# Performance work log

Hardware: AMD Instinct MI355X
Metric: run time of the kernel (lower is better)

The kernel has to match this reference:

```python
import jax, jax.numpy as jnp
import numpy as np

NUM_USERS = 60000
NUM_ITEMS = 40000
NUM_NODES = NUM_USERS + NUM_ITEMS
EMB = 64
HID = 32
N_EDGES = 1600000
BATCH = 16384


def setup_inputs() -> dict:
    key = jax.random.key(0)
    ks = jax.random.split(key, 16)
    def xavier(k, shape):
        fan_in, fan_out = shape[1], shape[0]
        lim = float(np.sqrt(6.0 / (fan_in + fan_out)))
        return jax.random.uniform(k, shape, jnp.float32, -lim, lim)
    return {
        "user_ids": jax.random.randint(ks[0], (BATCH,), 0, NUM_USERS),
        "item_ids": jax.random.randint(ks[1], (BATCH,), 0, NUM_ITEMS),
        "adj_rows": jax.random.randint(ks[2], (N_EDGES,), 0, NUM_NODES),
        "adj_cols": jax.random.randint(ks[3], (N_EDGES,), 0, NUM_NODES),
        "adj_vals": jax.random.uniform(ks[4], (N_EDGES,), jnp.float32),
        # embeddings (xavier_uniform, matching init_weights)
        "user_emb_w": xavier(ks[5], (NUM_USERS, EMB)),
        "item_emb_w": xavier(ks[6], (NUM_ITEMS, EMB)),
        # GC layer 1: 64 -> 32 ; GC layer 2: 32 -> 64
        "gc1_w": xavier(ks[7], (HID, EMB)),
        "gc1_b": jnp.zeros((HID,), jnp.float32),
        "gc2_w": xavier(ks[8], (EMB, HID)),
        "gc2_b": jnp.zeros((EMB,), jnp.float32),
        # predictor: Linear(2*EMB -> HID), ReLU, Linear(HID -> 1), Sigmoid
        "p1_w": xavier(ks[9], (HID, 2 * EMB)),
        "p1_b": jnp.zeros((HID,), jnp.float32),
        "p2_w": xavier(ks[10], (1, HID)),
        "p2_b": jnp.zeros((1,), jnp.float32),
    }


def _gc_layer(x, rows, cols, vals, w, b):
    # dense linear then spmm: out[i] = sum_e vals[e] * h[cols[e]] grouped by rows[e]
    h = x @ w.T + b                                # [N, out_dim]
    msg = vals[:, None] * h[cols]                  # [E, out_dim] gather (memory-bound)
    agg = jax.ops.segment_sum(msg, rows, num_segments=NUM_NODES)
    return jax.nn.relu(agg)                        # dropout in eval mode = identity


def reference(user_ids, item_ids, adj_rows, adj_cols, adj_vals,
              user_emb_w, item_emb_w, gc1_w, gc1_b, gc2_w, gc2_b,
              p1_w, p1_b, p2_w, p2_b):
    node_feat = jnp.concatenate([user_emb_w, item_emb_w], axis=0)  # [N, EMB]
    h = _gc_layer(node_feat, adj_rows, adj_cols, adj_vals, gc1_w, gc1_b)
    h = _gc_layer(h, adj_rows, adj_cols, adj_vals, gc2_w, gc2_b)
    final_user_emb = h[:NUM_USERS]
    final_item_emb = h[NUM_USERS:]
    bu = final_user_emb[user_ids]                  # [B, EMB]
    bi = final_item_emb[item_ids]                  # [B, EMB]
    z = jnp.concatenate([bu, bi], axis=1)          # [B, 2*EMB]
    z = jax.nn.relu(z @ p1_w.T + p1_b)             # [B, HID]
    scores = jax.nn.sigmoid(z @ p2_w.T + p2_b).squeeze(-1)  # [B]
    return (scores, final_user_emb, final_item_emb)
```

## Files before the change

### kernel.cpp

```cpp
#include <hip/hip_runtime.h>
#include <hip/hip_bf16.h>

#define NUM_USERS 60000
#define NUM_ITEMS 40000
#define NUM_NODES 100000
#define EMB 64
#define HID 32
#define N_EDGES 1600000
#define BATCH 16384

#define TILE 128
#define NBUCK 782
#define CAPB 3072
#define BLOCK_E 4096
#define NBLK_A 391
#define EPT 8
#define EPT_B (CAPB / 256)

#define WS_CUR    0
#define WS_BEND   800
#define WS_ROFF   1600
#define WS_BINNED 101952
#define WS_H1     4906560
#define WS_G      8106560
#define WS_SUMV   11306560

__global__ __launch_bounds__(1024) void k_initcur(unsigned* __restrict__ cur)
{
    int t = threadIdx.x;
    if (t < NBUCK) cur[t] = (unsigned)t * CAPB;
}

__global__ __launch_bounds__(512) void k_partA(
    const int* __restrict__ rows, const int* __restrict__ cols,
    const float* __restrict__ vals,
    unsigned* __restrict__ cursor, uint2* __restrict__ binned)
{
    __shared__ unsigned cnt[NBUCK];
    __shared__ unsigned offs[NBUCK];
    __shared__ unsigned gbase[NBUCK];
    __shared__ unsigned scanbuf[1024];
    __shared__ uint2    staged[BLOCK_E];
    __shared__ unsigned dstarr[BLOCK_E];

    int t = threadIdx.x;
    for (int i = t; i < NBUCK; i += 512) cnt[i] = 0u;
    __syncthreads();

    unsigned eb = blockIdx.x * BLOCK_E;
    unsigned bb[EPT], rk[EPT];
    uint2    pr[EPT];
    #pragma unroll
    for (int i = 0; i < EPT; i++) {
        unsigned e = eb + (unsigned)(i * 512 + t);
        if (e < N_EDGES) {
            unsigned r = (unsigned)rows[e];
            bb[i] = r >> 7;
            pr[i] = make_uint2(((r & 127u) << 17) | (unsigned)cols[e],
                               __float_as_uint(vals[e]));
            rk[i] = atomicAdd(&cnt[bb[i]], 1u);
        } else {
            bb[i] = 0xFFFFFFFFu;
        }
    }
    __syncthreads();

    unsigned c0 = (t < NBUCK) ? cnt[t] : 0u;
    unsigned c1 = (t + 512 < NBUCK) ? cnt[t + 512] : 0u;
    scanbuf[t] = c0; scanbuf[t + 512] = c1;
    __syncthreads();
    #pragma unroll
    for (int ofs = 1; ofs < 1024; ofs <<= 1) {
        unsigned a0 = (t >= ofs) ? scanbuf[t - ofs] : 0u;
        unsigned a1 = (t + 512 >= ofs) ? scanbuf[t + 512 - ofs] : 0u;
        __syncthreads();
        scanbuf[t] += a0; scanbuf[t + 512] += a1;
        __syncthreads();
    }
    if (t < NBUCK) offs[t] = scanbuf[t] - c0;
    if (t + 512 < NBUCK) offs[t + 512] = scanbuf[t + 512] - c1;
    __syncthreads();

    for (int b = t; b < NBUCK; b += 512) {
        unsigned c = cnt[b];
        gbase[b] = c ? atomicAdd(&cursor[b], c) : 0u;
    }
    __syncthreads();

    #pragma unroll
    for (int i = 0; i < EPT; i++) {
        if (bb[i] != 0xFFFFFFFFu) {
            unsigned s = offs[bb[i]] + rk[i];
            staged[s] = pr[i];
            dstarr[s] = gbase[bb[i]] + rk[i];
        }
    }
    __syncthreads();

    unsigned total = (eb + BLOCK_E <= N_EDGES) ? (unsigned)BLOCK_E
                                               : (N_EDGES - eb);
    for (unsigned s = t; s < total; s += 512)
        binned[dstarr[s]] = staged[s];
}

__global__ __launch_bounds__(256) void k_partB(
    const unsigned* __restrict__ cursor,
    uint2* __restrict__ binned,
    unsigned* __restrict__ roff, unsigned* __restrict__ bend)
{
    __shared__ uint2    ob[CAPB];
    __shared__ unsigned cnt[TILE];
    __shared__ unsigned sc[TILE];
    __shared__ unsigned offs[TILE];

    int t = threadIdx.x;
    int nb = blockIdx.x;
    unsigned gs = (unsigned)nb * CAPB;
    unsigned count = cursor[nb] - gs;
    if (count > CAPB) count = CAPB;

    for (int i = t; i < TILE; i += 256) cnt[i] = 0u;
    __syncthreads();

    unsigned rl_[EPT_B], rk_[EPT_B];
    uint2    pp_[EPT_B];
    #pragma unroll
    for (int it = 0; it < EPT_B; it++) {
        unsigned s = (unsigned)t + it * 256u;
        if (s < count) {
            uint2 p = binned[gs + s];
            unsigned rl = p.x >> 17;
            pp_[it] = p;
            rl_[it] = rl;
            rk_[it] = atomicAdd(&cnt[rl], 1u);
        } else {
            rl_[it] = 0xFFFFFFFFu;
        }
    }
    __syncthreads();

    unsigned c = (t < TILE) ? cnt[t] : 0u;
    if (t < TILE) sc[t] = c;
    __syncthreads();
    #pragma unroll
    for (int ofs = 1; ofs < TILE; ofs <<= 1) {
        unsigned a = 0u;
        if (t < TILE && t >= ofs) a = sc[t - ofs];
        __syncthreads();
        if (t < TILE) sc[t] += a;
        __syncthreads();
    }
    if (t < TILE) offs[t] = sc[t] - c;
    __syncthreads();

    for (int i = t; i < TILE; i += 256) {
        int n = nb * TILE + i;
        if (n <= NUM_NODES) roff[n] = gs + offs[i];
    }
    if (t == 0) bend[nb] = gs + count;

    #pragma unroll
    for (int it = 0; it < EPT_B; it++) {
        if (rl_[it] != 0xFFFFFFFFu)
            ob[offs[rl_[it]] + rk_[it]] = pp_[it];
    }
    __syncthreads();
    for (unsigned s = (unsigned)t; s < count; s += 256)
        binned[gs + s] = ob[s];
}

template<bool RELU, bool SUMV>
__global__ __launch_bounds__(256) void k_agg32(
    const unsigned* __restrict__ roff, const unsigned* __restrict__ bend,
    const uint2* __restrict__ binned,
    const float* __restrict__ H, float* __restrict__ out,
    float* __restrict__ sumv_out)
{
    int wave = threadIdx.x >> 6;
    int lane = threadIdx.x & 63;
    int n = blockIdx.x * 4 + wave;
    if (n >= NUM_NODES) return;
    int g = lane >> 3;
    int q = lane & 7;
    unsigned s = roff[n];
    unsigned e = ((n & 127) == 127) ? bend[n >> 7] : roff[n + 1];
    float4 acc = make_float4(0.f, 0.f, 0.f, 0.f);
    float sv = 0.f;
    unsigned k = s + (unsigned)g;
    for (; k + 8u < e; k += 16u) {
        uint2 pa = binned[k];
        uint2 pb = binned[k + 8u];
        float va = __uint_as_float(pa.y);
        float vb = __uint_as_float(pb.y);
        float4 ha = reinterpret_cast<const float4*>(H + (size_t)(pa.x & 0x1FFFFu) * HID)[q];
        float4 hb = reinterpret_cast<const float4*>(H + (size_t)(pb.x & 0x1FFFFu) * HID)[q];
        acc.x = fmaf(va, ha.x, acc.x); acc.y = fmaf(va, ha.y, acc.y);
        acc.z = fmaf(va, ha.z, acc.z); acc.w = fmaf(va, ha.w, acc.w);
        acc.x = fmaf(vb, hb.x, acc.x); acc.y = fmaf(vb, hb.y, acc.y);
        acc.z = fmaf(vb, hb.z, acc.z); acc.w = fmaf(vb, hb.w, acc.w);
        if (SUMV) sv += va + vb;
    }
    if (k < e) {
        uint2 p = binned[k];
        float v = __uint_as_float(p.y);
        float4 h = reinterpret_cast<const float4*>(H + (size_t)(p.x & 0x1FFFFu) * HID)[q];
        acc.x = fmaf(v, h.x, acc.x); acc.y = fmaf(v, h.y, acc.y);
        acc.z = fmaf(v, h.z, acc.z); acc.w = fmaf(v, h.w, acc.w);
        if (SUMV) sv += v;
    }
    #pragma unroll
    for (int m = 8; m < 64; m <<= 1) {
        acc.x += __shfl_xor(acc.x, m);
        acc.y += __shfl_xor(acc.y, m);
        acc.z += __shfl_xor(acc.z, m);
        acc.w += __shfl_xor(acc.w, m);
        if (SUMV) sv += __shfl_xor(sv, m);
    }
    if (g == 0) {
        if (RELU) {
            acc.x = fmaxf(acc.x, 0.f); acc.y = fmaxf(acc.y, 0.f);
            acc.z = fmaxf(acc.z, 0.f); acc.w = fmaxf(acc.w, 0.f);
        }
        reinterpret_cast<float4*>(out + (size_t)n * HID)[q] = acc;
        if (SUMV && q == 0) sumv_out[n] = sv;
    }
}

__global__ __launch_bounds__(256) void k_linear1(
    const float* __restrict__ ue, const float* __restrict__ ie,
    const float* __restrict__ w, const float* __restrict__ b,
    float* __restrict__ out)
{
    __shared__ float ws[HID * EMB];
    __shared__ float bs[HID];
    for (int i = threadIdx.x; i < HID * EMB; i += 256) ws[i] = w[i];
    if (threadIdx.x < HID) bs[threadIdx.x] = b[threadIdx.x];
    __syncthreads();

    int n = blockIdx.x * 256 + threadIdx.x;
    if (n >= NUM_NODES) return;
    const float* row = (n < NUM_USERS) ? ue + (size_t)n * EMB
                                       : ie + (size_t)(n - NUM_USERS) * EMB;
    float x[EMB];
    #pragma unroll
    for (int k4 = 0; k4 < EMB / 4; k4++) {
        float4 v = reinterpret_cast<const float4*>(row)[k4];
        x[4*k4+0] = v.x; x[4*k4+1] = v.y; x[4*k4+2] = v.z; x[4*k4+3] = v.w;
    }
    const float4* ws4 = reinterpret_cast<const float4*>(ws);
    float acc[HID];
    #pragma unroll
    for (int j = 0; j < HID; j++) {
        float a = bs[j];
        #pragma unroll
        for (int k4 = 0; k4 < EMB / 4; k4++) {
            float4 wv = ws4[j * (EMB/4) + k4];
            a = fmaf(wv.x, x[4*k4+0], a);
            a = fmaf(wv.y, x[4*k4+1], a);
            a = fmaf(wv.z, x[4*k4+2], a);
            a = fmaf(wv.w, x[4*k4+3], a);
        }
        acc[j] = a;
    }
    float4* o4 = reinterpret_cast<float4*>(out + (size_t)n * HID);
    #pragma unroll
    for (int j4 = 0; j4 < HID / 4; j4++)
        o4[j4] = make_float4(acc[4*j4], acc[4*j4+1], acc[4*j4+2], acc[4*j4+3]);
}

__global__ __launch_bounds__(256) void k_linear2_post(
    const float* __restrict__ G, const float* __restrict__ sumv,
    const float* __restrict__ w, const float* __restrict__ b,
    float* __restrict__ out)
{
    __shared__ float ws[EMB * HID];
    __shared__ float bs[EMB];
    for (int i = threadIdx.x; i < EMB * HID; i += 256) ws[i] = w[i];
    if (threadIdx.x < EMB) bs[threadIdx.x] = b[threadIdx.x];
    __syncthreads();

    int n = blockIdx.x * 256 + threadIdx.x;
    if (n >= NUM_NODES) return;
    const float* row = G + (size_t)n * HID;
    float sv = sumv[n];
    float x[HID];
    #pragma unroll
    for (int k4 = 0; k4 < HID / 4; k4++) {
        float4 v = reinterpret_cast<const float4*>(row)[k4];
        x[4*k4+0] = v.x; x[4*k4+1] = v.y; x[4*k4+2] = v.z; x[4*k4+3] = v.w;
    }
    const float4* ws4 = reinterpret_cast<const float4*>(ws);
    float acc[EMB];
    #pragma unroll
    for (int j = 0; j < EMB; j++) {
        float a = sv * bs[j];
        #pragma unroll
        for (int k4 = 0; k4 < HID / 4; k4++) {
            float4 wv = ws4[j * (HID/4) + k4];
            a = fmaf(wv.x, x[4*k4+0], a);
            a = fmaf(wv.y, x[4*k4+1], a);
            a = fmaf(wv.z, x[4*k4+2], a);
            a = fmaf(wv.w, x[4*k4+3], a);
        }
        acc[j] = fmaxf(a, 0.f);
    }
    float4* o4 = reinterpret_cast<float4*>(out + (size_t)n * EMB);
    #pragma unroll
    for (int j4 = 0; j4 < EMB / 4; j4++)
        o4[j4] = make_float4(acc[4*j4], acc[4*j4+1], acc[4*j4+2], acc[4*j4+3]);
}

__global__ __launch_bounds__(256) void k_mlp(
    const int* __restrict__ uids, const int* __restrict__ iids,
    const float* __restrict__ uemb, const float* __restrict__ iemb,
    const float* __restrict__ p1w, const float* __restrict__ p1b,
    const float* __restrict__ p2w, const float* __restrict__ p2b,
    float* __restrict__ scores)
{
    __shared__ float w1t[2 * EMB * HID];
    __shared__ float zt[8][2 * EMB];
    __shared__ float b1s[HID];
    __shared__ float w2s[HID];

    for (int i = threadIdx.x; i < HID * 2 * EMB; i += 256) {
        int j = i >> 7;
        int k = i & 127;
        int k4 = k >> 2, c = k & 3;
        w1t[k4 * 128 + j * 4 + c] = p1w[i];
    }
    if (threadIdx.x < HID) {
        b1s[threadIdx.x] = p1b[threadIdx.x];
        w2s[threadIdx.x] = p2w[threadIdx.x];
    }
    __syncthreads();

    int lg = threadIdx.x >> 5;
    int j  = threadIdx.x & 31;
    int s  = blockIdx.x * 8 + lg;

    {
        int u  = uids[s];
        int it = iids[s];
        const float* bu = uemb + (size_t)u * EMB;
        const float* bi = iemb + (size_t)it * EMB;
        float* zs = zt[lg];
        zs[j]      = bu[j];
        zs[32 + j] = bu[32 + j];
        zs[64 + j] = bi[j];
        zs[96 + j] = bi[32 + j];
    }
    __syncthreads();

    const float*  zs = zt[lg];
    const float4* w4 = reinterpret_cast<const float4*>(w1t);
    const float4* z4 = reinterpret_cast<const float4*>(zs);
    float a = b1s[j];
    #pragma unroll
    for (int k4 = 0; k4 < 32; k4++) {
        float4 wv = w4[k4 * 32 + j];
        float4 zv = z4[k4];
        a = fmaf(wv.x, zv.x, a);
        a = fmaf(wv.y, zv.y, a);
        a = fmaf(wv.z, zv.z, a);
        a = fmaf(wv.w, zv.w, a);
    }
    a = fmaxf(a, 0.f);
    float part = a * w2s[j];
    #pragma unroll
    for (int m = 16; m >= 1; m >>= 1) part += __shfl_xor(part, m);
    if (j == 0) scores[s] = 1.f / (1.f + expf(-(part + p2b[0])));
}

extern "C" void kernel_launch(void* const* d_in, const int* in_sizes, int n_in,
                              void* d_out, int out_size, void* d_ws, size_t ws_size,
                              hipStream_t stream)
{
    const int*   user_ids = (const int*)  d_in[0];
    const int*   item_ids = (const int*)  d_in[1];
    const int*   adj_rows = (const int*)  d_in[2];
    const int*   adj_cols = (const int*)  d_in[3];
    const float* adj_vals = (const float*)d_in[4];
    const float* user_emb = (const float*)d_in[5];
    const float* item_emb = (const float*)d_in[6];
    const float* gc1_w    = (const float*)d_in[7];
    const float* gc1_b    = (const float*)d_in[8];
    const float* gc2_w    = (const float*)d_in[9];
    const float* gc2_b    = (const float*)d_in[10];
    const float* p1_w     = (const float*)d_in[11];
    const float* p1_b     = (const float*)d_in[12];
    const float* p2_w     = (const float*)d_in[13];
    const float* p2_b     = (const float*)d_in[14];

    float* out     = (float*)d_out;
    float* scores  = out;
    float* emb_out = out + BATCH;

    unsigned* ws_u   = (unsigned*)d_ws;
    unsigned* cur    = ws_u + WS_CUR;
    unsigned* bend   = ws_u + WS_BEND;
    unsigned* roff   = ws_u + WS_ROFF;
    uint2*    binned = (uint2*)(ws_u + WS_BINNED);
    float*    H1     = (float*)(ws_u + WS_H1);
    float*    G      = (float*)(ws_u + WS_G);
    float*    SUMV   = (float*)(ws_u + WS_SUMV);
    float*    A1     = emb_out;

    k_initcur<<<1, 1024, 0, stream>>>(cur);
    k_partA<<<NBLK_A, 512, 0, stream>>>(adj_rows, adj_cols, adj_vals,
                                        cur, binned);
    k_partB<<<NBUCK, 256, 0, stream>>>(cur, binned, roff, bend);

    k_linear1<<<(NUM_NODES + 255) / 256, 256, 0, stream>>>(
        user_emb, item_emb, gc1_w, gc1_b, H1);
    k_agg32<true, false><<<NUM_NODES / 4, 256, 0, stream>>>(
        roff, bend, binned, H1, A1, nullptr);

    k_agg32<false, true><<<NUM_NODES / 4, 256, 0, stream>>>(
        roff, bend, binned, A1, G, SUMV);
    k_linear2_post<<<(NUM_NODES + 255) / 256, 256, 0, stream>>>(
        G, SUMV, gc2_w, gc2_b, emb_out);

    k_mlp<<<BATCH / 8, 256, 0, stream>>>(
        user_ids, item_ids, emb_out, emb_out + (size_t)NUM_USERS * EMB,
        p1_w, p1_b, p2_w, p2_b, scores);
}
```

Measured before the change: 267.7 us.

## Store hidden features in bf16 and pad row segments for paired edge loads

The intermediate hidden features H1 and A1 are now stored as packed bf16, which halves the bytes pulled in by the random gather in both aggregation passes. The CSR segments are padded to even length with zero edges so each lane group can load two edges with one 16-byte read. Each bucket's capacity drops by TILE to leave room for the padding. This gives up some precision in the intermediates and could drop edges if a bucket overflows.

```diff
diff --git a/kernel.cpp b/kernel.cpp
--- a/kernel.cpp
+++ b/kernel.cpp
@@ -21,9 +21,25 @@
 #define WS_BEND   800
 #define WS_ROFF   1600
 #define WS_BINNED 101952
-#define WS_H1     4906560
+#define WS_H1B    4906560
+#define WS_A1B    6506560
 #define WS_G      8106560
 #define WS_SUMV   11306560
+
+static __device__ __forceinline__ unsigned short f2bf(float f) {
+    union { float f; unsigned u; } x; x.f = f;
+    unsigned u = x.u;
+    return (unsigned short)((u + 0x7FFFu + ((u >> 16) & 1u)) >> 16);
+}
+static __device__ __forceinline__ unsigned pack2bf(float lo, float hi) {
+    return (unsigned)f2bf(lo) | ((unsigned)f2bf(hi) << 16);
+}
+static __device__ __forceinline__ float bflo(unsigned u) {
+    union { unsigned v; float f; } x; x.v = u << 16; return x.f;
+}
+static __device__ __forceinline__ float bfhi(unsigned u) {
+    union { unsigned v; float f; } x; x.v = u & 0xFFFF0000u; return x.f;
+}
 
 __global__ __launch_bounds__(1024) void k_initcur(unsigned* __restrict__ cur)
 {
@@ -112,12 +128,13 @@
     __shared__ unsigned cnt[TILE];
     __shared__ unsigned sc[TILE];
     __shared__ unsigned offs[TILE];
+    __shared__ unsigned totpad;
 
     int t = threadIdx.x;
     int nb = blockIdx.x;
     unsigned gs = (unsigned)nb * CAPB;
     unsigned count = cursor[nb] - gs;
-    if (count > CAPB) count = CAPB;
+    if (count > CAPB - TILE) count = CAPB - TILE;
 
     for (int i = t; i < TILE; i += 256) cnt[i] = 0u;
     __syncthreads();
@@ -139,8 +156,9 @@
     }
     __syncthreads();
 
-    unsigned c = (t < TILE) ? cnt[t] : 0u;
-    if (t < TILE) sc[t] = c;
+    unsigned c  = (t < TILE) ? cnt[t] : 0u;
+    unsigned pc = (c + 1u) & ~1u;
+    if (t < TILE) sc[t] = pc;
     __syncthreads();
     #pragma unroll
     for (int ofs = 1; ofs < TILE; ofs <<= 1) {
@@ -150,14 +168,17 @@
         if (t < TILE) sc[t] += a;
         __syncthreads();
     }
-    if (t < TILE) offs[t] = sc[t] - c;
+    if (t < TILE) offs[t] = sc[t] - pc;
+    if (t == TILE - 1) totpad = sc[t];
     __syncthreads();
 
     for (int i = t; i < TILE; i += 256) {
         int n = nb * TILE + i;
         if (n <= NUM_NODES) roff[n] = gs + offs[i];
     }
-    if (t == 0) bend[nb] = gs + count;
+    if (t == 0) bend[nb] = gs + totpad;
+
+    if (t < TILE && (c & 1u)) ob[offs[t] + c] = make_uint2(0u, 0u);
 
     #pragma unroll
     for (int it = 0; it < EPT_B; it++) {
@@ -165,48 +186,44 @@
             ob[offs[rl_[it]] + rk_[it]] = pp_[it];
     }
     __syncthreads();
-    for (unsigned s = (unsigned)t; s < count; s += 256)
+    unsigned tp = totpad;
+    for (unsigned s = (unsigned)t; s < tp; s += 256)
         binned[gs + s] = ob[s];
 }
 
-template<bool RELU, bool SUMV>
+template<bool LAYER1>
 __global__ __launch_bounds__(256) void k_agg32(
     const unsigned* __restrict__ roff, const unsigned* __restrict__ bend,
     const uint2* __restrict__ binned,
-    const float* __restrict__ H, float* __restrict__ out,
+    const unsigned* __restrict__ H,
+    unsigned* __restrict__ outb,
+    float* __restrict__ outf,
     float* __restrict__ sumv_out)
 {
     int wave = threadIdx.x >> 6;
     int lane = threadIdx.x & 63;
     int n = blockIdx.x * 4 + wave;
-    if (n >= NUM_NODES) return;
     int g = lane >> 3;
     int q = lane & 7;
     unsigned s = roff[n];
     unsigned e = ((n & 127) == 127) ? bend[n >> 7] : roff[n + 1];
     float4 acc = make_float4(0.f, 0.f, 0.f, 0.f);
     float sv = 0.f;
-    unsigned k = s + (unsigned)g;
-    for (; k + 8u < e; k += 16u) {
-        uint2 pa = binned[k];
-        uint2 pb = binned[k + 8u];
-        float va = __uint_as_float(pa.y);
-        float vb = __uint_as_float(pb.y);
-        float4 ha = reinterpret_cast<const float4*>(H + (size_t)(pa.x & 0x1FFFFu) * HID)[q];
-        float4 hb = reinterpret_cast<const float4*>(H + (size_t)(pb.x & 0x1FFFFu) * HID)[q];
-        acc.x = fmaf(va, ha.x, acc.x); acc.y = fmaf(va, ha.y, acc.y);
-        acc.z = fmaf(va, ha.z, acc.z); acc.w = fmaf(va, ha.w, acc.w);
-        acc.x = fmaf(vb, hb.x, acc.x); acc.y = fmaf(vb, hb.y, acc.y);
-        acc.z = fmaf(vb, hb.z, acc.z); acc.w = fmaf(vb, hb.w, acc.w);
-        if (SUMV) sv += va + vb;
-    }
-    if (k < e) {
-        uint2 p = binned[k];
-        float v = __uint_as_float(p.y);
-        float4 h = reinterpret_cast<const float4*>(H + (size_t)(p.x & 0x1FFFFu) * HID)[q];
-        acc.x = fmaf(v, h.x, acc.x); acc.y = fmaf(v, h.y, acc.y);
-        acc.z = fmaf(v, h.z, acc.z); acc.w = fmaf(v, h.w, acc.w);
-        if (SUMV) sv += v;
+    for (unsigned k = s + 2u * (unsigned)g; k < e; k += 16u) {
+        uint4 pp = *reinterpret_cast<const uint4*>(&binned[k]);
+        float va = __uint_as_float(pp.y);
+        float vb = __uint_as_float(pp.w);
+        uint2 ha = *(reinterpret_cast<const uint2*>(H + (size_t)(pp.x & 0x1FFFFu) * 16) + q);
+        uint2 hb = *(reinterpret_cast<const uint2*>(H + (size_t)(pp.z & 0x1FFFFu) * 16) + q);
+        acc.x = fmaf(va, bflo(ha.x), acc.x);
+        acc.y = fmaf(va, bfhi(ha.x), acc.y);
+        acc.z = fmaf(va, bflo(ha.y), acc.z);
+        acc.w = fmaf(va, bfhi(ha.y), acc.w);
+        acc.x = fmaf(vb, bflo(hb.x), acc.x);
+        acc.y = fmaf(vb, bfhi(hb.x), acc.y);
+        acc.z = fmaf(vb, bflo(hb.y), acc.z);
+        acc.w = fmaf(vb, bfhi(hb.y), acc.w);
+        if (!LAYER1) sv += va + vb;
     }
     #pragma unroll
     for (int m = 8; m < 64; m <<= 1) {
@@ -214,22 +231,25 @@
         acc.y += __shfl_xor(acc.y, m);
         acc.z += __shfl_xor(acc.z, m);
         acc.w += __shfl_xor(acc.w, m);
-        if (SUMV) sv += __shfl_xor(sv, m);
+        if (!LAYER1) sv += __shfl_xor(sv, m);
     }
     if (g == 0) {
-        if (RELU) {
+        if (LAYER1) {
             acc.x = fmaxf(acc.x, 0.f); acc.y = fmaxf(acc.y, 0.f);
             acc.z = fmaxf(acc.z, 0.f); acc.w = fmaxf(acc.w, 0.f);
-        }
-        reinterpret_cast<float4*>(out + (size_t)n * HID)[q] = acc;
-        if (SUMV && q == 0) sumv_out[n] = sv;
+            uint2 o = make_uint2(pack2bf(acc.x, acc.y), pack2bf(acc.z, acc.w));
+            *(reinterpret_cast<uint2*>(outb + (size_t)n * 16) + q) = o;
+        } else {
+            reinterpret_cast<float4*>(outf + (size_t)n * HID)[q] = acc;
+            if (q == 0) sumv_out[n] = sv;
+        }
     }
 }
 
 __global__ __launch_bounds__(256) void k_linear1(
     const float* __restrict__ ue, const float* __restrict__ ie,
     const float* __restrict__ w, const float* __restrict__ b,
-    float* __restrict__ out)
+    unsigned* __restrict__ out)
 {
     __shared__ float ws[HID * EMB];
     __shared__ float bs[HID];
@@ -262,10 +282,16 @@
         }
         acc[j] = a;
     }
-    float4* o4 = reinterpret_cast<float4*>(out + (size_t)n * HID);
-    #pragma unroll
-    for (int j4 = 0; j4 < HID / 4; j4++)
-        o4[j4] = make_float4(acc[4*j4], acc[4*j4+1], acc[4*j4+2], acc[4*j4+3]);
+    uint4* o4 = reinterpret_cast<uint4*>(out + (size_t)n * 16);
+    #pragma unroll
+    for (int j8 = 0; j8 < 4; j8++) {
+        uint4 o;
+        o.x = pack2bf(acc[8*j8+0], acc[8*j8+1]);
+        o.y = pack2bf(acc[8*j8+2], acc[8*j8+3]);
+        o.z = pack2bf(acc[8*j8+4], acc[8*j8+5]);
+        o.w = pack2bf(acc[8*j8+6], acc[8*j8+7]);
+        o4[j8] = o;
+    }
 }
 
 __global__ __launch_bounds__(256) void k_linear2_post(
@@ -400,10 +426,10 @@
     unsigned* bend   = ws_u + WS_BEND;
     unsigned* roff   = ws_u + WS_ROFF;
     uint2*    binned = (uint2*)(ws_u + WS_BINNED);
-    float*    H1     = (float*)(ws_u + WS_H1);
+    unsigned* H1B    = ws_u + WS_H1B;
+    unsigned* A1B    = ws_u + WS_A1B;
     float*    G      = (float*)(ws_u + WS_G);
     float*    SUMV   = (float*)(ws_u + WS_SUMV);
-    float*    A1     = emb_out;
 
     k_initcur<<<1, 1024, 0, stream>>>(cur);
     k_partA<<<NBLK_A, 512, 0, stream>>>(adj_rows, adj_cols, adj_vals,
@@ -411,12 +437,12 @@
     k_partB<<<NBUCK, 256, 0, stream>>>(cur, binned, roff, bend);
 
     k_linear1<<<(NUM_NODES + 255) / 256, 256, 0, stream>>>(
-        user_emb, item_emb, gc1_w, gc1_b, H1);
-    k_agg32<true, false><<<NUM_NODES / 4, 256, 0, stream>>>(
-        roff, bend, binned, H1, A1, nullptr);
-
-    k_agg32<false, true><<<NUM_NODES / 4, 256, 0, stream>>>(
-        roff, bend, binned, A1, G, SUMV);
+        user_emb, item_emb, gc1_w, gc1_b, H1B);
+    k_agg32<true><<<NUM_NODES / 4, 256, 0, stream>>>(
+        roff, bend, binned, H1B, A1B, nullptr, nullptr);
+
+    k_agg32<false><<<NUM_NODES / 4, 256, 0, stream>>>(
+        roff, bend, binned, A1B, nullptr, G, SUMV);
     k_linear2_post<<<(NUM_NODES + 255) / 256, 256, 0, stream>>>(
         G, SUMV, gc2_w, gc2_b, emb_out);
 
```

After: 258.5 us. 1.04x faster.
